# Kernel tuning notes

Hardware: AMD Instinct MI355X
Metric: run time of the kernel (lower is better)

## Reference

```python
import jax, jax.numpy as jnp
import numpy as np

N, M, D = 65536, 1024, 2


def setup_inputs() -> dict:
    key = jax.random.key(0)
    k1, k2, k3 = jax.random.split(key, 3)
    sample = jax.random.uniform(k1, (N, D), dtype=jnp.float32)
    mu = jax.random.uniform(k2, (M, D), dtype=jnp.float32)
    # original init: A = 10 * I; add small noise so covariances are anisotropic
    A = 10.0 * jnp.broadcast_to(jnp.eye(D, dtype=jnp.float32), (M, D, D)) \
        + 0.1 * jax.random.normal(k3, (M, D, D), dtype=jnp.float32)
    w = jnp.ones((M, 1), dtype=jnp.float32)
    return {"sample": sample, "mu": mu, "A": A, "w": w}


def reference(sample, mu, A, w):
    # gamma_j = A_j @ A_j^T  -> precision matrices, (M, D, D)
    gamma = jnp.einsum('mde,mfe->mdf', A, A)
    # 2x2 determinant (only case implemented in the original module)
    det = gamma[:, 0, 0] * gamma[:, 1, 1] - gamma[:, 0, 1] * gamma[:, 1, 0]
    # log weights: log_softmax(w) + 0.5 * log det(gamma)
    log_w = jax.nn.log_softmax(w[:, 0], axis=0) + 0.5 * jnp.log(det)  # (M,)
    # Mahalanobis quadratic form q_ij = (x_i - mu_j)^T gamma_j (x_i - mu_j),
    # expanded to avoid materializing an (N, M, D) difference tensor.
    xGx = jnp.einsum('nd,mde,ne->nm', sample, gamma, sample)          # (N, M)
    gm = jnp.einsum('mde,me->md', gamma, mu)                          # (M, D)
    cross = sample @ gm.T                                             # (N, M)
    mGm = jnp.einsum('md,md->m', gm, mu)                              # (M,)
    q = xGx - 2.0 * cross + mGm[None, :]
    # log-likelihood per sample: logsumexp_j (log_w_j - q_ij)
    return jax.nn.logsumexp(log_w[None, :] - q, axis=1)               # (N,)
```

## Files before the change

kernel.cpp:

```cpp
#include <hip/hip_runtime.h>
#include <math.h>

#define LOG2E 1.4426950408889634f
#define LN2   0.6931471805599453f

static constexpr int M = 1024;
static constexpr int N = 65536;


__device__ inline float wave_max64(float v) {
    #pragma unroll
    for (int o = 32; o > 0; o >>= 1) v = fmaxf(v, __shfl_xor(v, o));
    return v;
}
__device__ inline float wave_sum64(float v) {
    #pragma unroll
    for (int o = 32; o > 0; o >>= 1) v += __shfl_xor(v, o);
    return v;
}

__global__ __launch_bounds__(1024)
void gm_prep(const float* __restrict__ mu,
             const float* __restrict__ A,
             const float* __restrict__ w,
             float* __restrict__ ws) {
    __shared__ float r[16];
    const int j    = threadIdx.x;
    const int lane = j & 63;
    const int wv   = j >> 6;

    const float4 a = ((const float4*)A)[j];
    const float g00 = a.x*a.x + a.y*a.y;
    const float g01 = a.x*a.z + a.y*a.w;
    const float g11 = a.z*a.z + a.w*a.w;
    const float2 m  = ((const float2*)mu)[j];
    const float gm0 = g00*m.x + g01*m.y;
    const float gm1 = g01*m.x + g11*m.y;
    const float mGm = gm0*m.x + gm1*m.y;
    const float det = g00*g11 - g01*g01;
    const float wj  = w[j];

    float t = wave_max64(wj);
    if (lane == 0) r[wv] = t;
    __syncthreads();
    float wmax = r[0];
    #pragma unroll
    for (int i = 1; i < 16; i++) wmax = fmaxf(wmax, r[i]);
    __syncthreads();

    t = wave_sum64(expf(wj - wmax));
    if (lane == 0) r[wv] = t;
    __syncthreads();
    float se = 0.0f;
    #pragma unroll
    for (int i = 0; i < 16; i++) se += r[i];
    const float lse = wmax + logf(se);
    __syncthreads();

    const float log_w = wj - lse + 0.5f * logf(det);

    t = wave_max64(log_w);
    if (lane == 0) r[wv] = t;
    __syncthreads();
    float L = r[0];
    #pragma unroll
    for (int i = 1; i < 16; i++) L = fmaxf(L, r[i]);

    float* c = ws + j*8;
    c[0] = LOG2E * (log_w - mGm - L);
    c[1] = LOG2E * 2.0f * gm0;
    c[2] = LOG2E * 2.0f * gm1;
    c[3] = -LOG2E * g00;
    c[4] = -LOG2E * 2.0f * g01;
    c[5] = -LOG2E * g11;
    c[6] = 0.0f;
    c[7] = 0.0f;
    if (j == 0) ws[M*8] = LOG2E * L;
}

__global__ __launch_bounds__(1024)
void gm_main(const float* __restrict__ sample,
             const float* __restrict__ ws,
             float* __restrict__ out) {
    __shared__ __align__(16) float coef[M*8];
    __shared__ float partial[16*256];
    const int t = threadIdx.x;

    const float4* wsv = (const float4*)ws;
    float4* cv = (float4*)coef;
    cv[t]        = wsv[t];
    cv[t + 1024] = wsv[t + 1024];
    __syncthreads();

    const int lane = t & 63;
    const int wave = t >> 6;
    const int base = blockIdx.x * 256;

    float x0[4], x1[4], xx[4], xy[4], yy[4], acc[4];
    #pragma unroll
    for (int k = 0; k < 4; k++) {
        const float2 p = ((const float2*)sample)[base + 64*k + lane];
        x0[k] = p.x; x1[k] = p.y;
        xx[k] = p.x*p.x; xy[k] = p.x*p.y; yy[k] = p.y*p.y;
        acc[k] = 0.0f;
    }

    const float* c = coef + wave*64*8;
    #pragma unroll 4
    for (int jj = 0; jj < 64; jj++) {
        const float* cc = c + jj*8;
        const float c0 = cc[0], c1 = cc[1], c2 = cc[2];
        const float c3 = cc[3], c4 = cc[4], c5 = cc[5];
        #pragma unroll
        for (int k = 0; k < 4; k++) {
            const float v = fmaf(c5, yy[k],
                            fmaf(c4, xy[k],
                            fmaf(c3, xx[k],
                            fmaf(c2, x1[k],
                            fmaf(c1, x0[k], c0)))));
            acc[k] += __builtin_amdgcn_exp2f(v);
        }
    }

    #pragma unroll
    for (int k = 0; k < 4; k++)
        partial[wave*256 + 64*k + lane] = acc[k];
    __syncthreads();

    if (t < 256) {
        float s = 0.0f;
        #pragma unroll
        for (int w2 = 0; w2 < 16; w2++) s += partial[w2*256 + t];
        out[base + t] = LN2 * (ws[M*8] + __builtin_amdgcn_logf(s));
    }
}

__global__ __launch_bounds__(256)
void gm_fused(const float* __restrict__ sample,
              const float* __restrict__ mu,
              const float* __restrict__ A,
              const float* __restrict__ w,
              float* __restrict__ out) {
    __shared__ __align__(16) float coef[M*8];
    __shared__ float red[256];
    const int t = threadIdx.x;

    float wv[4], c0t[4], c1t[4], c2t[4], c3t[4], c4t[4], c5t[4];
    float wmaxl = -3.4e38f;
    #pragma unroll
    for (int k = 0; k < 4; k++) { wv[k] = w[t + 256*k]; wmaxl = fmaxf(wmaxl, wv[k]); }
    red[t] = wmaxl; __syncthreads();
    for (int off = 128; off > 0; off >>= 1) {
        if (t < off) red[t] = fmaxf(red[t], red[t+off]);
        __syncthreads();
    }
    const float wmax = red[0]; __syncthreads();
    float se = 0.0f;
    #pragma unroll
    for (int k = 0; k < 4; k++) se += expf(wv[k] - wmax);
    red[t] = se; __syncthreads();
    for (int off = 128; off > 0; off >>= 1) {
        if (t < off) red[t] = red[t] + red[t+off];
        __syncthreads();
    }
    const float lse = wmax + logf(red[0]); __syncthreads();

    float Lml = -3.4e38f;
    #pragma unroll
    for (int k = 0; k < 4; k++) {
        const int j = t + 256*k;
        const float4 a = ((const float4*)A)[j];
        const float g00 = a.x*a.x + a.y*a.y;
        const float g01 = a.x*a.z + a.y*a.w;
        const float g11 = a.z*a.z + a.w*a.w;
        const float2 m  = ((const float2*)mu)[j];
        const float gm0 = g00*m.x + g01*m.y;
        const float gm1 = g01*m.x + g11*m.y;
        const float mGm = gm0*m.x + gm1*m.y;
        const float det = g00*g11 - g01*g01;
        const float lw  = wv[k] - lse + 0.5f*logf(det);
        Lml = fmaxf(Lml, lw);
        c0t[k] = lw - mGm; c1t[k] = 2.0f*gm0; c2t[k] = 2.0f*gm1;
        c3t[k] = -g00; c4t[k] = -2.0f*g01; c5t[k] = -g11;
    }
    red[t] = Lml; __syncthreads();
    for (int off = 128; off > 0; off >>= 1) {
        if (t < off) red[t] = fmaxf(red[t], red[t+off]);
        __syncthreads();
    }
    const float L = red[0];
    #pragma unroll
    for (int k = 0; k < 4; k++) {
        float* c = coef + (t + 256*k)*8;
        c[0] = LOG2E*(c0t[k] - L); c[1] = LOG2E*c1t[k]; c[2] = LOG2E*c2t[k];
        c[3] = LOG2E*c3t[k]; c[4] = LOG2E*c4t[k]; c[5] = LOG2E*c5t[k];
    }
    __syncthreads();

    const int i = blockIdx.x*256 + t;
    const float2 xy = ((const float2*)sample)[i];
    const float x0 = xy.x, x1 = xy.y;
    const float xx = x0*x0, xyp = x0*x1, yy = x1*x1;
    float s0 = 0.0f, s1 = 0.0f;
    #pragma unroll 8
    for (int jj = 0; jj < M; jj++) {
        const float* cc = coef + jj*8;
        const float v = fmaf(cc[5], yy,
                        fmaf(cc[4], xyp,
                        fmaf(cc[3], xx,
                        fmaf(cc[2], x1,
                        fmaf(cc[1], x0, cc[0])))));
        const float e = __builtin_amdgcn_exp2f(v);
        if (jj & 1) s1 += e; else s0 += e;
    }
    out[i] = LN2 * (LOG2E*L + __builtin_amdgcn_logf(s0 + s1));
}

extern "C" void kernel_launch(void* const* d_in, const int* in_sizes, int n_in,
                              void* d_out, int out_size, void* d_ws, size_t ws_size,
                              hipStream_t stream) {
    const float* sample = (const float*)d_in[0];
    const float* mu     = (const float*)d_in[1];
    const float* A      = (const float*)d_in[2];
    const float* w      = (const float*)d_in[3];
    float* out = (float*)d_out;

    if (ws_size >= (size_t)(M*8 + 1) * sizeof(float)) {
        gm_prep<<<1, 1024, 0, stream>>>(mu, A, w, (float*)d_ws);
        gm_main<<<N/256, 1024, 0, stream>>>(sample, (const float*)d_ws, out);
    } else {
        gm_fused<<<N/256, 256, 0, stream>>>(sample, mu, A, w, out);
    }
}
```

Before: 76.32 us.

## Read wave-uniform coefficients from global memory as scalar loads, drop LDS staging

The main kernel no longer stages the coefficient table in LDS. Each wave gets a uniform index through readfirstlane, so it can read its 128 components straight from global memory, likely as scalar loads. Blocks shrink to 512 threads covering 64 samples with one sample per lane, instead of 1024 threads covering 256 samples with four per lane, which gives four times as many blocks and a smaller partial-sum reduction. The change removes LDS traffic and the per-block table copy. In exchange each lane keeps fewer independent samples in flight, leaving less work per coefficient load, and many more blocks each re-read the table through the cache.

```diff
diff --git a/kernel.cpp b/kernel.cpp
--- a/kernel.cpp
+++ b/kernel.cpp
@@ -78,60 +78,50 @@
     if (j == 0) ws[M*8] = LOG2E * L;
 }
 
-__global__ __launch_bounds__(1024)
+__global__ __launch_bounds__(512)
 void gm_main(const float* __restrict__ sample,
              const float* __restrict__ ws,
              float* __restrict__ out) {
-    __shared__ __align__(16) float coef[M*8];
-    __shared__ float partial[16*256];
-    const int t = threadIdx.x;
-
-    const float4* wsv = (const float4*)ws;
-    float4* cv = (float4*)coef;
-    cv[t]        = wsv[t];
-    cv[t + 1024] = wsv[t + 1024];
-    __syncthreads();
-
+    __shared__ float partial[8*64];
+    const int t    = threadIdx.x;
     const int lane = t & 63;
-    const int wave = t >> 6;
-    const int base = blockIdx.x * 256;
-
-    float x0[4], x1[4], xx[4], xy[4], yy[4], acc[4];
-    #pragma unroll
-    for (int k = 0; k < 4; k++) {
-        const float2 p = ((const float2*)sample)[base + 64*k + lane];
-        x0[k] = p.x; x1[k] = p.y;
-        xx[k] = p.x*p.x; xy[k] = p.x*p.y; yy[k] = p.y*p.y;
-        acc[k] = 0.0f;
-    }
-
-    const float* c = coef + wave*64*8;
+    const int wv   = __builtin_amdgcn_readfirstlane(t >> 6);
+
+    const int i = blockIdx.x*64 + lane;
+    const float2 p = ((const float2*)sample)[i];
+    const float x0 = p.x, x1 = p.y;
+    const float xx = x0*x0, xy = x0*x1, yy = x1*x1;
+
+    const float* __restrict__ c = ws + (size_t)wv * 128 * 8;
+
+    float a0 = 0.0f, a1 = 0.0f, a2 = 0.0f, a3 = 0.0f;
     #pragma unroll 4
-    for (int jj = 0; jj < 64; jj++) {
-        const float* cc = c + jj*8;
-        const float c0 = cc[0], c1 = cc[1], c2 = cc[2];
-        const float c3 = cc[3], c4 = cc[4], c5 = cc[5];
-        #pragma unroll
-        for (int k = 0; k < 4; k++) {
-            const float v = fmaf(c5, yy[k],
-                            fmaf(c4, xy[k],
-                            fmaf(c3, xx[k],
-                            fmaf(c2, x1[k],
-                            fmaf(c1, x0[k], c0)))));
-            acc[k] += __builtin_amdgcn_exp2f(v);
-        }
-    }
-
-    #pragma unroll
-    for (int k = 0; k < 4; k++)
-        partial[wave*256 + 64*k + lane] = acc[k];
-    __syncthreads();
-
-    if (t < 256) {
+    for (int jj = 0; jj < 128; jj += 4) {
+        const float* ca = c + (jj+0)*8;
+        const float* cb = c + (jj+1)*8;
+        const float* cc = c + (jj+2)*8;
+        const float* cd = c + (jj+3)*8;
+        const float va = fmaf(ca[5], yy, fmaf(ca[4], xy, fmaf(ca[3], xx,
+                         fmaf(ca[2], x1, ca[1]*x0)))) + ca[0];
+        const float vb = fmaf(cb[5], yy, fmaf(cb[4], xy, fmaf(cb[3], xx,
+                         fmaf(cb[2], x1, cb[1]*x0)))) + cb[0];
+        const float vc = fmaf(cc[5], yy, fmaf(cc[4], xy, fmaf(cc[3], xx,
+                         fmaf(cc[2], x1, cc[1]*x0)))) + cc[0];
+        const float vd = fmaf(cd[5], yy, fmaf(cd[4], xy, fmaf(cd[3], xx,
+                         fmaf(cd[2], x1, cd[1]*x0)))) + cd[0];
+        a0 += __builtin_amdgcn_exp2f(va);
+        a1 += __builtin_amdgcn_exp2f(vb);
+        a2 += __builtin_amdgcn_exp2f(vc);
+        a3 += __builtin_amdgcn_exp2f(vd);
+    }
+    partial[wv*64 + lane] = (a0 + a1) + (a2 + a3);
+    __syncthreads();
+
+    if (t < 64) {
         float s = 0.0f;
         #pragma unroll
-        for (int w2 = 0; w2 < 16; w2++) s += partial[w2*256 + t];
-        out[base + t] = LN2 * (ws[M*8] + __builtin_amdgcn_logf(s));
+        for (int w2 = 0; w2 < 8; w2++) s += partial[w2*64 + t];
+        out[blockIdx.x*64 + t] = LN2 * (ws[M*8] + __builtin_amdgcn_logf(s));
     }
 }
 
@@ -198,18 +188,15 @@
     __syncthreads();
 
     const int i = blockIdx.x*256 + t;
-    const float2 xy = ((const float2*)sample)[i];
-    const float x0 = xy.x, x1 = xy.y;
+    const float2 xyv = ((const float2*)sample)[i];
+    const float x0 = xyv.x, x1 = xyv.y;
     const float xx = x0*x0, xyp = x0*x1, yy = x1*x1;
     float s0 = 0.0f, s1 = 0.0f;
     #pragma unroll 8
     for (int jj = 0; jj < M; jj++) {
         const float* cc = coef + jj*8;
-        const float v = fmaf(cc[5], yy,
-                        fmaf(cc[4], xyp,
-                        fmaf(cc[3], xx,
-                        fmaf(cc[2], x1,
-                        fmaf(cc[1], x0, cc[0])))));
+        const float v = fmaf(cc[5], yy, fmaf(cc[4], xyp, fmaf(cc[3], xx,
+                        fmaf(cc[2], x1, fmaf(cc[1], x0, cc[0])))));
         const float e = __builtin_amdgcn_exp2f(v);
         if (jj & 1) s1 += e; else s0 += e;
     }
@@ -227,7 +214,7 @@
 
     if (ws_size >= (size_t)(M*8 + 1) * sizeof(float)) {
         gm_prep<<<1, 1024, 0, stream>>>(mu, A, w, (float*)d_ws);
-        gm_main<<<N/256, 1024, 0, stream>>>(sample, (const float*)d_ws, out);
+        gm_main<<<N/64, 512, 0, stream>>>(sample, (const float*)d_ws, out);
     } else {
         gm_fused<<<N/256, 256, 0, stream>>>(sample, mu, A, w, out);
     }
```

New measurement: 82.09 us. +7.6%, slower.

## Fuse coefficient prep into main kernel and pack coefficients as float4 triples

Applied to the files above, without the earlier changes.

Replaces the two-kernel prep+main pipeline with a single kernel in which every block recomputes the per-component coefficients and softmax reductions in shared memory. This removes a launch and the round trip through workspace memory. Coefficients are packed 6 per component and read as three float4 loads per component pair, cutting shared-memory load instructions. The cost is redundant prep work (A, mu, w loads plus three block reductions) repeated in each of the 256 blocks.

```diff
diff --git a/kernel.cpp b/kernel.cpp
--- a/kernel.cpp
+++ b/kernel.cpp
@@ -6,7 +6,6 @@
 
 static constexpr int M = 1024;
 static constexpr int N = 65536;
-
 
 __device__ inline float wave_max64(float v) {
     #pragma unroll
@@ -20,200 +19,107 @@
 }
 
 __global__ __launch_bounds__(1024)
-void gm_prep(const float* __restrict__ mu,
-             const float* __restrict__ A,
-             const float* __restrict__ w,
-             float* __restrict__ ws) {
-    __shared__ float r[16];
-    const int j    = threadIdx.x;
-    const int lane = j & 63;
-    const int wv   = j >> 6;
+void gm_all(const float* __restrict__ sample,
+            const float* __restrict__ mu,
+            const float* __restrict__ A,
+            const float* __restrict__ w,
+            float* __restrict__ out) {
+    __shared__ __align__(16) float coef[M*6];
+    __shared__ float partial[16*256];
+    __shared__ float red[16];
 
-    const float4 a = ((const float4*)A)[j];
+    const int t    = threadIdx.x;
+    const int lane = t & 63;
+    const int wv   = t >> 6;
+    const int base = blockIdx.x * 256;
+
+    float x0[4], x1[4];
+    #pragma unroll
+    for (int k = 0; k < 4; k++) {
+        const float2 p = ((const float2*)sample)[base + 64*k + lane];
+        x0[k] = p.x; x1[k] = p.y;
+    }
+
+    const float4 a = ((const float4*)A)[t];
     const float g00 = a.x*a.x + a.y*a.y;
     const float g01 = a.x*a.z + a.y*a.w;
     const float g11 = a.z*a.z + a.w*a.w;
-    const float2 m  = ((const float2*)mu)[j];
+    const float2 m  = ((const float2*)mu)[t];
     const float gm0 = g00*m.x + g01*m.y;
     const float gm1 = g01*m.x + g11*m.y;
     const float mGm = gm0*m.x + gm1*m.y;
     const float det = g00*g11 - g01*g01;
-    const float wj  = w[j];
+    const float wj  = w[t];
 
-    float t = wave_max64(wj);
-    if (lane == 0) r[wv] = t;
+    float r = wave_max64(wj);
+    if (lane == 0) red[wv] = r;
     __syncthreads();
-    float wmax = r[0];
+    float wmax = red[0];
     #pragma unroll
-    for (int i = 1; i < 16; i++) wmax = fmaxf(wmax, r[i]);
+    for (int i = 1; i < 16; i++) wmax = fmaxf(wmax, red[i]);
     __syncthreads();
 
-    t = wave_sum64(expf(wj - wmax));
-    if (lane == 0) r[wv] = t;
+    r = wave_sum64(expf(wj - wmax));
+    if (lane == 0) red[wv] = r;
     __syncthreads();
     float se = 0.0f;
     #pragma unroll
-    for (int i = 0; i < 16; i++) se += r[i];
+    for (int i = 0; i < 16; i++) se += red[i];
     const float lse = wmax + logf(se);
     __syncthreads();
 
     const float log_w = wj - lse + 0.5f * logf(det);
 
-    t = wave_max64(log_w);
-    if (lane == 0) r[wv] = t;
+    r = wave_max64(log_w);
+    if (lane == 0) red[wv] = r;
     __syncthreads();
-    float L = r[0];
+    float L = red[0];
     #pragma unroll
-    for (int i = 1; i < 16; i++) L = fmaxf(L, r[i]);
+    for (int i = 1; i < 16; i++) L = fmaxf(L, red[i]);
 
-    float* c = ws + j*8;
+    float* c = coef + t*6;
     c[0] = LOG2E * (log_w - mGm - L);
     c[1] = LOG2E * 2.0f * gm0;
     c[2] = LOG2E * 2.0f * gm1;
     c[3] = -LOG2E * g00;
     c[4] = -LOG2E * 2.0f * g01;
     c[5] = -LOG2E * g11;
-    c[6] = 0.0f;
-    c[7] = 0.0f;
-    if (j == 0) ws[M*8] = LOG2E * L;
-}
-
-__global__ __launch_bounds__(1024)
-void gm_main(const float* __restrict__ sample,
-             const float* __restrict__ ws,
-             float* __restrict__ out) {
-    __shared__ __align__(16) float coef[M*8];
-    __shared__ float partial[16*256];
-    const int t = threadIdx.x;
-
-    const float4* wsv = (const float4*)ws;
-    float4* cv = (float4*)coef;
-    cv[t]        = wsv[t];
-    cv[t + 1024] = wsv[t + 1024];
     __syncthreads();
 
-    const int lane = t & 63;
-    const int wave = t >> 6;
-    const int base = blockIdx.x * 256;
+    const float xx[4] = {x0[0]*x0[0], x0[1]*x0[1], x0[2]*x0[2], x0[3]*x0[3]};
+    const float xy[4] = {x0[0]*x1[0], x0[1]*x1[1], x0[2]*x1[2], x0[3]*x1[3]};
+    const float yy[4] = {x1[0]*x1[0], x1[1]*x1[1], x1[2]*x1[2], x1[3]*x1[3]};
+    float acc[4] = {0.0f, 0.0f, 0.0f, 0.0f};
 
-    float x0[4], x1[4], xx[4], xy[4], yy[4], acc[4];
-    #pragma unroll
-    for (int k = 0; k < 4; k++) {
-        const float2 p = ((const float2*)sample)[base + 64*k + lane];
-        x0[k] = p.x; x1[k] = p.y;
-        xx[k] = p.x*p.x; xy[k] = p.x*p.y; yy[k] = p.y*p.y;
-        acc[k] = 0.0f;
-    }
-
-    const float* c = coef + wave*64*8;
+    const float4* cw = (const float4*)(coef + wv*64*6);
     #pragma unroll 4
-    for (int jj = 0; jj < 64; jj++) {
-        const float* cc = c + jj*8;
-        const float c0 = cc[0], c1 = cc[1], c2 = cc[2];
-        const float c3 = cc[3], c4 = cc[4], c5 = cc[5];
+    for (int jj = 0; jj < 32; jj++) {
+        const float4 q0 = cw[jj*3 + 0];
+        const float4 q1 = cw[jj*3 + 1];
+        const float4 q2 = cw[jj*3 + 2];
         #pragma unroll
         for (int k = 0; k < 4; k++) {
-            const float v = fmaf(c5, yy[k],
-                            fmaf(c4, xy[k],
-                            fmaf(c3, xx[k],
-                            fmaf(c2, x1[k],
-                            fmaf(c1, x0[k], c0)))));
-            acc[k] += __builtin_amdgcn_exp2f(v);
+            const float va = fmaf(q1.y, yy[k], fmaf(q1.x, xy[k],
+                             fmaf(q0.w, xx[k], fmaf(q0.z, x1[k],
+                             fmaf(q0.y, x0[k], q0.x)))));
+            const float vb = fmaf(q2.w, yy[k], fmaf(q2.z, xy[k],
+                             fmaf(q2.y, xx[k], fmaf(q2.x, x1[k],
+                             fmaf(q1.w, x0[k], q1.z)))));
+            acc[k] += __builtin_amdgcn_exp2f(va) + __builtin_amdgcn_exp2f(vb);
         }
     }
 
     #pragma unroll
     for (int k = 0; k < 4; k++)
-        partial[wave*256 + 64*k + lane] = acc[k];
+        partial[wv*256 + 64*k + lane] = acc[k];
     __syncthreads();
 
     if (t < 256) {
         float s = 0.0f;
         #pragma unroll
         for (int w2 = 0; w2 < 16; w2++) s += partial[w2*256 + t];
-        out[base + t] = LN2 * (ws[M*8] + __builtin_amdgcn_logf(s));
+        out[base + t] = LN2 * (LOG2E*L + __builtin_amdgcn_logf(s));
     }
-}
-
-__global__ __launch_bounds__(256)
-void gm_fused(const float* __restrict__ sample,
-              const float* __restrict__ mu,
-              const float* __restrict__ A,
-              const float* __restrict__ w,
-              float* __restrict__ out) {
-    __shared__ __align__(16) float coef[M*8];
-    __shared__ float red[256];
-    const int t = threadIdx.x;
-
-    float wv[4], c0t[4], c1t[4], c2t[4], c3t[4], c4t[4], c5t[4];
-    float wmaxl = -3.4e38f;
-    #pragma unroll
-    for (int k = 0; k < 4; k++) { wv[k] = w[t + 256*k]; wmaxl = fmaxf(wmaxl, wv[k]); }
-    red[t] = wmaxl; __syncthreads();
-    for (int off = 128; off > 0; off >>= 1) {
-        if (t < off) red[t] = fmaxf(red[t], red[t+off]);
-        __syncthreads();
-    }
-    const float wmax = red[0]; __syncthreads();
-    float se = 0.0f;
-    #pragma unroll
-    for (int k = 0; k < 4; k++) se += expf(wv[k] - wmax);
-    red[t] = se; __syncthreads();
-    for (int off = 128; off > 0; off >>= 1) {
-        if (t < off) red[t] = red[t] + red[t+off];
-        __syncthreads();
-    }
-    const float lse = wmax + logf(red[0]); __syncthreads();
-
-    float Lml = -3.4e38f;
-    #pragma unroll
-    for (int k = 0; k < 4; k++) {
-        const int j = t + 256*k;
-        const float4 a = ((const float4*)A)[j];
-        const float g00 = a.x*a.x + a.y*a.y;
-        const float g01 = a.x*a.z + a.y*a.w;
-        const float g11 = a.z*a.z + a.w*a.w;
-        const float2 m  = ((const float2*)mu)[j];
-        const float gm0 = g00*m.x + g01*m.y;
-        const float gm1 = g01*m.x + g11*m.y;
-        const float mGm = gm0*m.x + gm1*m.y;
-        const float det = g00*g11 - g01*g01;
-        const float lw  = wv[k] - lse + 0.5f*logf(det);
-        Lml = fmaxf(Lml, lw);
-        c0t[k] = lw - mGm; c1t[k] = 2.0f*gm0; c2t[k] = 2.0f*gm1;
-        c3t[k] = -g00; c4t[k] = -2.0f*g01; c5t[k] = -g11;
-    }
-    red[t] = Lml; __syncthreads();
-    for (int off = 128; off > 0; off >>= 1) {
-        if (t < off) red[t] = fmaxf(red[t], red[t+off]);
-        __syncthreads();
-    }
-    const float L = red[0];
-    #pragma unroll
-    for (int k = 0; k < 4; k++) {
-        float* c = coef + (t + 256*k)*8;
-        c[0] = LOG2E*(c0t[k] - L); c[1] = LOG2E*c1t[k]; c[2] = LOG2E*c2t[k];
-        c[3] = LOG2E*c3t[k]; c[4] = LOG2E*c4t[k]; c[5] = LOG2E*c5t[k];
-    }
-    __syncthreads();
-
-    const int i = blockIdx.x*256 + t;
-    const float2 xy = ((const float2*)sample)[i];
-    const float x0 = xy.x, x1 = xy.y;
-    const float xx = x0*x0, xyp = x0*x1, yy = x1*x1;
-    float s0 = 0.0f, s1 = 0.0f;
-    #pragma unroll 8
-    for (int jj = 0; jj < M; jj++) {
-        const float* cc = coef + jj*8;
-        const float v = fmaf(cc[5], yy,
-                        fmaf(cc[4], xyp,
-                        fmaf(cc[3], xx,
-                        fmaf(cc[2], x1,
-                        fmaf(cc[1], x0, cc[0])))));
-        const float e = __builtin_amdgcn_exp2f(v);
-        if (jj & 1) s1 += e; else s0 += e;
-    }
-    out[i] = LN2 * (LOG2E*L + __builtin_amdgcn_logf(s0 + s1));
 }
 
 extern "C" void kernel_launch(void* const* d_in, const int* in_sizes, int n_in,
@@ -224,11 +130,7 @@
     const float* A      = (const float*)d_in[2];
     const float* w      = (const float*)d_in[3];
     float* out = (float*)d_out;
+    (void)d_ws; (void)ws_size;
 
-    if (ws_size >= (size_t)(M*8 + 1) * sizeof(float)) {
-        gm_prep<<<1, 1024, 0, stream>>>(mu, A, w, (float*)d_ws);
-        gm_main<<<N/256, 1024, 0, stream>>>(sample, (const float*)d_ws, out);
-    } else {
-        gm_fused<<<N/256, 256, 0, stream>>>(sample, mu, A, w, out);
-    }
+    gm_all<<<N/256, 1024, 0, stream>>>(sample, mu, A, w, out);
 }
```

Result: faster. 74.44 us (-2.5%).
